# Optimization experiments

Measured on AMD Instinct MI355X. Metric: run time of the kernel, lower is better.

Reference implementation:

```python
import jax, jax.numpy as jnp
import numpy as np

B, T, F, H = 64, 1024, 160, 1024


def setup_inputs() -> dict:
    key = jax.random.key(0)
    ks = jax.random.split(key, 18)
    s = lambda k, shape, scale=0.05: (jax.random.normal(k, shape, jnp.float32) * scale)
    inp = {
        "x": jax.random.normal(ks[0], (B, T, F), jnp.float32),
        # encoder GRU layer 0 (input F -> hidden H), PyTorch gate order r,z,n
        "Wih0": s(ks[1], (3 * H, F)), "Whh0": s(ks[2], (3 * H, H)),
        "bih0": s(ks[3], (3 * H,)), "bhh0": s(ks[4], (3 * H,)),
        # encoder GRU layer 1 (input H -> hidden H)
        "Wih1": s(ks[5], (3 * H, H)), "Whh1": s(ks[6], (3 * H, H)),
        "bih1": s(ks[7], (3 * H,)), "bhh1": s(ks[8], (3 * H,)),
        # fc: (n_enc_layers*H) -> H
        "fcW": s(ks[9], (H, 2 * H)), "fcb": jnp.zeros((H,), jnp.float32),
        # decoder GRUCell (input F -> hidden H)
        "dWih": s(ks[10], (3 * H, F)), "dWhh": s(ks[11], (3 * H, H)),
        "dbih": s(ks[12], (3 * H,)), "dbhh": s(ks[13], (3 * H,)),
        # dec_proj: H -> F
        "pW": s(ks[14], (F, H)), "pb": jnp.zeros((F,), jnp.float32),
    }
    return inp


def gru_step(h, xt, Wih, Whh, bih, bhh):
    # PyTorch GRU/GRUCell math, gate order (r, z, n)
    gi = xt @ Wih.T + bih          # [B, 3H]
    gh = h @ Whh.T + bhh           # [B, 3H]
    ir, iz, inn = jnp.split(gi, 3, axis=-1)
    hr, hz, hn = jnp.split(gh, 3, axis=-1)
    r = jax.nn.sigmoid(ir + hr)
    z = jax.nn.sigmoid(iz + hz)
    n = jnp.tanh(inn + r * hn)
    return (1.0 - z) * n + z * h


def reference(x, Wih0, Whh0, bih0, bhh0, Wih1, Whh1, bih1, bhh1,
              fcW, fcb, dWih, dWhh, dbih, dbhh, pW, pb):
    Bx, Tx = x.shape[0], x.shape[1]
    xs = jnp.swapaxes(x, 0, 1)  # [T, B, F]

    def run_layer(seq, Wih, Whh, bih, bhh):
        h0 = jnp.zeros((Bx, Whh.shape[1]), x.dtype)
        def step(h, xt):
            h = gru_step(h, xt, Wih, Whh, bih, bhh)
            return h, h
        hT, hs = jax.lax.scan(step, h0, seq)
        return hT, hs

    # 2-layer encoder GRU (dropout disabled: eval-mode / deterministic reference)
    h1, hs0 = run_layer(xs, Wih0, Whh0, bih0, bhh0)
    h2, _ = run_layer(hs0, Wih1, Whh1, bih1, bhh1)

    # h_n permute+view -> concat(layer0, layer1) along features
    h = jnp.tanh(jnp.concatenate([h1, h2], axis=-1) @ fcW.T + fcb)  # [B, H]

    i0 = jnp.zeros((Bx, pW.shape[0]), x.dtype)
    def dec_step(carry, _):
        hd, i = carry
        hd = gru_step(hd, i, dWih, dWhh, dbih, dbhh)
        i = hd @ pW.T + pb
        return (hd, i), i
    _, outs = jax.lax.scan(dec_step, (h, i0), None, length=Tx)  # [T, B, F]
    return jnp.swapaxes(outs, 0, 1)  # [B, T, F]
```

## Files before the change

kernel.cpp:

```cpp
#include <hip/hip_runtime.h>
#include <math.h>

#define NWG 256
#define NTH 512

typedef _Float16 f16;
typedef __attribute__((ext_vector_type(8))) _Float16 h8;
typedef __attribute__((ext_vector_type(4))) float f4;

namespace {
constexpr int T_ = 1024, F_ = 160, H_ = 1024;
constexpr float SC = 2048.f;
constexpr float INV = 1.f / 2048.f;

constexpr int ESLOTH = 512 * 64 * 8;
constexpr int DSLOTH = 256 * 64 * 8;
constexpr int ELO = 256;
constexpr int DLO = 128;

constexpr size_t WS_BAR  = 0;
constexpr size_t WS_CVEC = 4096;
constexpr size_t WS_WDEC = 16384;
constexpr size_t WS_ENCA = WS_WDEC + (size_t)4 * H_ * H_ * 4;
constexpr size_t WS_DECA = WS_ENCA + (size_t)2 * ESLOTH * 2;
constexpr size_t WS_STRM = WS_DECA + (size_t)2 * DSLOTH * 2;

constexpr int DBUF_B = 135168;
constexpr int TBUF_B = DBUF_B + 17408;
constexpr int ZP_B   = TBUF_B + 2048;
constexpr int LDS_B  = ZP_B + 64;
}

__device__ __forceinline__ f4 MF(h8 a, h8 b, f4 c) {
  return __builtin_amdgcn_mfma_f32_16x16x32_f16(a, b, c, 0, 0, 0);
}

__device__ __forceinline__ void fsplit(float v, f16& hi, f16& lo) {
  const float hf = (fabsf(v) >= 6.103515625e-05f) ? (float)(f16)v : 0.f;
  hi = (f16)hf;
  lo = (f16)((v - hf) * SC);
}

__device__ __forceinline__ void gbar(unsigned* bar, int wg, unsigned& phase) {
  __syncthreads();
  ++phase;
  if (threadIdx.x == 0) {
    unsigned* grp = bar + ((wg >> 4) << 5);
    unsigned old = __hip_atomic_fetch_add(grp, 1u, __ATOMIC_ACQ_REL, __HIP_MEMORY_SCOPE_AGENT);
    if ((old & 15u) == 15u) {
      unsigned r = __hip_atomic_fetch_add(bar + 512, 1u, __ATOMIC_ACQ_REL, __HIP_MEMORY_SCOPE_AGENT);
      if ((r & 15u) == 15u)
        __hip_atomic_fetch_add(bar + 544, 1u, __ATOMIC_ACQ_REL, __HIP_MEMORY_SCOPE_AGENT);
    }
    while (__hip_atomic_load(bar + 544, __ATOMIC_RELAXED, __HIP_MEMORY_SCOPE_AGENT) < phase)
      __builtin_amdgcn_s_sleep(1);
    (void)__hip_atomic_load(bar + 544, __ATOMIC_ACQUIRE, __HIP_MEMORY_SCOPE_AGENT);
  }
  __syncthreads();
}

__device__ void stageEnc(f16* __restrict__ whi, f16* __restrict__ wlo,
                         const float* __restrict__ Wx, const float* __restrict__ Wh,
                         int KX, int XOo, int KO, int u0, int tid) {
  for (int task = tid; task < KO * 24; task += NTH) {
    const int oct = task / 24;
    const int sl = task - oct * 24;
    const int g = (sl < 16) ? (sl >> 3) : 2;
    const int u = u0 + (sl & 7);
    const float* src = (oct < XOo)
        ? (Wx + (size_t)(g * H_ + u) * KX + (size_t)oct * 8)
        : (Wh + (size_t)(g * H_ + u) * H_ + (size_t)(oct - XOo) * 8);
    const float4 a = *(const float4*)src;
    const float4 b = *(const float4*)(src + 4);
    const float v[8] = {a.x, a.y, a.z, a.w, b.x, b.y, b.z, b.w};
    h8 hv, lv;
#pragma unroll
    for (int e = 0; e < 8; ++e) { f16 hh, ll; fsplit(v[e], hh, ll); hv[e] = hh; lv[e] = ll; }
    *(h8*)(whi + ((size_t)oct * 25 + sl) * 8) = hv;
    if (wlo) *(h8*)(wlo + ((size_t)oct * 25 + sl) * 8) = lv;
  }
}

__device__ void stageDec(f16* __restrict__ whi, f16* __restrict__ wlo,
                         const float* __restrict__ wdec, const float* __restrict__ dWhh,
                         int u0, int tid, bool t1set) {
  for (int task = tid; task < 128 * 32; task += NTH) {
    const int oct = task >> 5, sl = task & 31;
    const int g = sl >> 3;
    const int u = u0 + (sl & 7);
    float v[8];
    if (t1set) {
      if (g == 2) {
#pragma unroll
        for (int e = 0; e < 8; ++e) v[e] = 0.f;
      } else {
        const float* s = dWhh + (size_t)((g == 3 ? 2 : g) * H_ + u) * H_ + (size_t)oct * 8;
        const float4 a = *(const float4*)s, b = *(const float4*)(s + 4);
        v[0]=a.x; v[1]=a.y; v[2]=a.z; v[3]=a.w; v[4]=b.x; v[5]=b.y; v[6]=b.z; v[7]=b.w;
      }
    } else {
      const float* s = wdec + (size_t)(g * H_ + u) * H_ + (size_t)oct * 8;
      const float4 a = *(const float4*)s, b = *(const float4*)(s + 4);
      v[0]=a.x; v[1]=a.y; v[2]=a.z; v[3]=a.w; v[4]=b.x; v[5]=b.y; v[6]=b.z; v[7]=b.w;
    }
    h8 hv, lv;
#pragma unroll
    for (int e = 0; e < 8; ++e) { f16 hh, ll; fsplit(v[e], hh, ll); hv[e] = hh; lv[e] = ll; }
    *(h8*)(whi + ((size_t)oct * 33 + sl) * 8) = hv;
    *(h8*)(wlo + ((size_t)oct * 33 + sl) * 8) = lv;
  }
}

__device__ void stageProj(f16* __restrict__ whi, f16* __restrict__ wlo,
                          const float* __restrict__ pW, int f0, int tid) {
  for (int task = tid; task < 128 * 16; task += NTH) {
    const int oct = task >> 4, sl = task & 15;
    const float* s = pW + (size_t)(f0 + sl) * H_ + (size_t)oct * 8;
    const float4 a = *(const float4*)s, b = *(const float4*)(s + 4);
    const float v[8] = {a.x, a.y, a.z, a.w, b.x, b.y, b.z, b.w};
    h8 hv, lv;
#pragma unroll
    for (int e = 0; e < 8; ++e) { f16 hh, ll; fsplit(v[e], hh, ll); hv[e] = hh; lv[e] = ll; }
    *(h8*)(whi + ((size_t)oct * 17 + sl) * 8) = hv;
    *(h8*)(wlo + ((size_t)oct * 17 + sl) * 8) = lv;
  }
}

template<int NT, bool NSPLIT, int ROWH, bool STRM>
__device__ __forceinline__ void gmm(f4* Dh, f4* Dc,
    const f16* __restrict__ Ab, int aoctBase, int loOct,
    const f16* __restrict__ whi, const f16* __restrict__ wlo,
    const f16* __restrict__ strm,
    int ktn, int octBase, int XO, int ls, int lq, int lane,
    const f16* __restrict__ zp) {
  auto LD = [&](int kk, h8& ah, h8& al, h8& bh0, h8& bl0, h8& bh1, h8& bl1) {
    const int aoct = aoctBase + kk * 4 + lq;
    ah = *(const h8*)(Ab + (size_t)aoct * 512);
    al = *(const h8*)(Ab + (size_t)(aoct + loOct) * 512);
    const int oct = octBase + kk * 4 + lq;
    bh0 = *(const h8*)(whi + ((size_t)oct * ROWH + ls) * 8);
    if constexpr (STRM) bl0 = *(const h8*)(strm + ((size_t)(kk * 2) * 64 + lane) * 8);
    else bl0 = *(const h8*)(wlo + ((size_t)oct * ROWH + ls) * 8);
    if constexpr (NT == 2) {
      bool act = true; int psl;
      if constexpr (NSPLIT) { act = (ls < 8) ? (oct < XO) : (oct >= XO); psl = 16 + (ls & 7); }
      else { psl = 16 + ls; }
      bh1 = *(const h8*)(act ? (whi + ((size_t)oct * ROWH + psl) * 8) : zp);
      if constexpr (STRM) bl1 = *(const h8*)(strm + ((size_t)(kk * 2 + 1) * 64 + lane) * 8);
      else bl1 = *(const h8*)(act ? (wlo + ((size_t)oct * ROWH + psl) * 8) : zp);
    }
  };
  h8 ah, al, bh0, bl0, bh1, bl1;
  LD(0, ah, al, bh0, bl0, bh1, bl1);
  for (int kk = 0; kk < ktn; ++kk) {
    h8 ah2, al2, bh02, bl02, bh12, bl12;
    const int nk = (kk + 1 < ktn) ? (kk + 1) : kk;
    LD(nk, ah2, al2, bh02, bl02, bh12, bl12);
    Dh[0] = MF(ah, bh0, Dh[0]);
    Dc[0] = MF(al, bh0, Dc[0]);
    Dc[0] = MF(ah, bl0, Dc[0]);
    if constexpr (NT == 2) {
      Dh[1] = MF(ah, bh1, Dh[1]);
      Dc[1] = MF(al, bh1, Dc[1]);
      Dc[1] = MF(ah, bl1, Dc[1]);
    }
    ah = ah2; al = al2; bh0 = bh02; bl0 = bl02;
    if constexpr (NT == 2) { bh1 = bh12; bl1 = bl12; }
  }
}

__device__ __forceinline__ void gmm_x(f4* Dh, f4* Dc, const float* __restrict__ xp,
    const f16* __restrict__ whi, const f16* __restrict__ wlo,
    int ls, int lq, const f16* __restrict__ zp) {
#pragma unroll
  for (int kk = 0; kk < 5; ++kk) {
    const float4 a = *(const float4*)(xp + kk * 32);
    const float4 b = *(const float4*)(xp + kk * 32 + 4);
    const float v[8] = {a.x, a.y, a.z, a.w, b.x, b.y, b.z, b.w};
    h8 ah, al;
#pragma unroll
    for (int e = 0; e < 8; ++e) { f16 hh, ll; fsplit(v[e], hh, ll); ah[e] = hh; al[e] = ll; }
    const int oct = kk * 4 + lq;
    {
      const h8 bh2 = *(const h8*)(whi + ((size_t)oct * 25 + ls) * 8);
      const h8 bl2 = *(const h8*)(wlo + ((size_t)oct * 25 + ls) * 8);
      Dh[0] = MF(ah, bh2, Dh[0]);
      Dc[0] = MF(al, bh2, Dc[0]);
      Dc[0] = MF(ah, bl2, Dc[0]);
    }
    {
      const bool act = (ls < 8);
      const int psl = 16 + (ls & 7);
      const h8 bh2 = *(const h8*)(act ? (whi + ((size_t)oct * 25 + psl) * 8) : zp);
      const h8 bl2 = *(const h8*)(act ? (wlo + ((size_t)oct * 25 + psl) * 8) : zp);
      Dh[1] = MF(ah, bh2, Dh[1]);
      Dc[1] = MF(al, bh2, Dc[1]);
      Dc[1] = MF(ah, bl2, Dc[1]);
    }
  }
}

__global__ void build_c_kernel(const float* __restrict__ dWih, const float* __restrict__ dbih,
                               const float* __restrict__ pb, float* __restrict__ cvec) {
  const int r = blockIdx.x * 256 + threadIdx.x;
  if (r >= 3 * H_) return;
  float a = dbih[r];
  for (int f = 0; f < F_; ++f) a += dWih[(size_t)r * F_ + f] * pb[f];
  cvec[r] = a;
}

__global__ void build_wdec_kernel(const float* __restrict__ dWih, const float* __restrict__ dWhh,
                                  const float* __restrict__ pW, float* __restrict__ wdec) {
  const int idx = blockIdx.x * 256 + threadIdx.x;
  if (idx >= 3 * H_ * 128) return;
  const int row = idx >> 7;
  const int oct = idx & 127;
  float v[8] = {0, 0, 0, 0, 0, 0, 0, 0};
  const float* wr = dWih + (size_t)row * F_;
  for (int f = 0; f < F_; ++f) {
    const float w = wr[f];
    const float4 p0 = *(const float4*)(pW + (size_t)f * H_ + oct * 8);
    const float4 p1 = *(const float4*)(pW + (size_t)f * H_ + oct * 8 + 4);
    v[0] += w * p0.x; v[1] += w * p0.y; v[2] += w * p0.z; v[3] += w * p0.w;
    v[4] += w * p1.x; v[5] += w * p1.y; v[6] += w * p1.z; v[7] += w * p1.w;
  }
  if ((row >> 10) < 2) {
    const float* hr = dWhh + (size_t)row * H_ + oct * 8;
#pragma unroll
    for (int e = 0; e < 8; ++e) v[e] += hr[e];
  }
  float* o = wdec + (size_t)row * H_ + oct * 8;
#pragma unroll
  for (int e = 0; e < 8; ++e) o[e] = v[e];
}
__global__ void build_wdec_nh(const float* __restrict__ dWhh, float* __restrict__ wdec) {
  const int idx = blockIdx.x * 256 + threadIdx.x;
  if (idx >= H_ * H_) return;
  wdec[(size_t)3 * H_ * H_ + idx] = dWhh[(size_t)2 * H_ * H_ + idx];
}

__global__ void build_strm(const float* __restrict__ Wih1, const float* __restrict__ Whh1,
                           f16* __restrict__ strm) {
  const size_t idx = (size_t)blockIdx.x * 256 + threadIdx.x;
  const int j = (int)(idx & 7);
  const int lane = (int)((idx >> 3) & 63);
  const int nt = (int)((idx >> 9) & 1);
  const int kk = (int)((idx >> 10) & 31);
  const int kb = (int)((idx >> 15) & 1);
  const int wg = (int)(idx >> 16);
  const int c = lane & 15, lq = lane >> 4;
  const int oct = kb * 128 + kk * 4 + lq;
  const int k = oct * 8 + j;
  float v = 0.f;
  if (nt == 0) {
    const int row = (c >> 3) * H_ + wg * 8 + (c & 7);
    v = (oct < 128) ? Wih1[(size_t)row * H_ + k] : Whh1[(size_t)row * H_ + (k - 1024)];
  } else {
    const bool act = (c < 8) ? (oct < 128) : (oct >= 128);
    if (act) {
      const int row = 2 * H_ + wg * 8 + (c & 7);
      v = (oct < 128) ? Wih1[(size_t)row * H_ + k] : Whh1[(size_t)row * H_ + (k - 1024)];
    }
  }
  f16 hh, ll; fsplit(v, hh, ll);
  strm[idx] = ll;
}

__global__ void __launch_bounds__(NTH, 1) speech_ae_persistent(
    const float* __restrict__ x,
    const float* __restrict__ Wih0, const float* __restrict__ Whh0,
    const float* __restrict__ bih0, const float* __restrict__ bhh0,
    const float* __restrict__ Wih1, const float* __restrict__ Whh1,
    const float* __restrict__ bih1, const float* __restrict__ bhh1,
    const float* __restrict__ fcW, const float* __restrict__ fcb,
    const float* __restrict__ dbih, const float* __restrict__ dbhh,
    const float* __restrict__ pW, const float* __restrict__ pb,
    const float* __restrict__ dWhh,
    float* __restrict__ out, void* ws) {
  extern __shared__ char ldsb[];
  f16* wh = (f16*)ldsb;
  float* dbuf = (float*)(ldsb + DBUF_B);
  float* tbuf = (float*)(ldsb + TBUF_B);
  f16* zp = (f16*)(ldsb + ZP_B);

  char* wsb = (char*)ws;
  unsigned* bar = (unsigned*)(wsb + WS_BAR);
  const float* cvec = (const float*)(wsb + WS_CVEC);
  const float* wdec = (const float*)(wsb + WS_WDEC);
  f16* encA = (f16*)(wsb + WS_ENCA);
  f16* decA = (f16*)(wsb + WS_DECA);
  const f16* strm = (const f16*)(wsb + WS_STRM);

  const int tid = threadIdx.x, wg = blockIdx.x;
  const int lane = tid & 63, wv = tid >> 6;
  const int ls = lane & 15, lq = lane >> 4;
  const int m0 = (wv & 3) * 16, kb = wv >> 2;
  const int mb = m0 + ls;
  const bool isL1 = (wg < 128);
  unsigned phase = 0;
  const f16* strmW = strm + (size_t)(wg * 2 + kb) * 32768;

  const float* bi = isL1 ? bih1 : bih0;
  const float* bh_ = isL1 ? bhh1 : bhh0;
  const int eru = (isL1 ? wg * 8 : (wg - 128) * 8) + wv;
  const float ebr = bi[eru] + bh_[eru];
  const float ebz = bi[H_ + eru] + bh_[H_ + eru];
  const float ebni = bi[2 * H_ + eru];
  const float ebnh = bh_[2 * H_ + eru];
  float hreg = 0.f;

  float b1r = 0, b1z = 0, b1ni = 0, b1nh = 0, bfr = 0, bfz = 0, bfni = 0, bfnh = 0, hdreg = 0.f;
  if (wg < 128) {
    const int rw = wg * 8 + wv;
    b1r = dbih[rw] + dbhh[rw];
    b1z = dbih[H_ + rw] + dbhh[H_ + rw];
    b1ni = dbih[2 * H_ + rw];
    b1nh = dbhh[2 * H_ + rw];
    bfr = cvec[rw] + dbhh[rw];
    bfz = cvec[H_ + rw] + dbhh[H_ + rw];
    bfni = cvec[2 * H_ + rw];
    bfnh = dbhh[2 * H_ + rw];
  }
  const int f0 = (wg - 128) * 16;
  float pbr[4] = {0, 0, 0, 0};
  if (wg >= 128 && wg < 138 && tid < 256) {
    const int fq = tid & 3;
#pragma unroll
    for (int e = 0; e < 4; ++e) pbr[e] = pb[f0 + fq * 4 + e];
  }

  if (isL1) stageEnc(wh, nullptr, Wih1, Whh1, H_, 128, 256, wg * 8, tid);
  else stageEnc(wh, wh + 29600, Wih0, Whh0, F_, 20, 148, (wg - 128) * 8, tid);
  if (tid < 16) zp[tid] = (f16)0.f;
  __syncthreads();

  for (int s = 0; s <= T_; ++s) {
    const bool active = isL1 ? (s >= 1) : (s < T_);
    if (active) {
      const int t = isL1 ? (s - 1) : s;
      f4 Dh[2] = {{0.f,0.f,0.f,0.f},{0.f,0.f,0.f,0.f}};
      f4 Dc[2] = {{0.f,0.f,0.f,0.f},{0.f,0.f,0.f,0.f}};
      if (isL1) {
        if (kb == 0) {
          const f16* Ab = encA + (size_t)(t & 1) * ESLOTH + (size_t)mb * 8;
          gmm<2, true, 25, true>(Dh, Dc, Ab, 0, ELO, wh, nullptr, strmW, 32, 0, 128, ls, lq, lane, zp);
        } else if (t >= 1) {
          const f16* Ab = encA + (size_t)((t - 1) & 1) * ESLOTH + (size_t)mb * 8;
          gmm<2, true, 25, true>(Dh, Dc, Ab, 128, ELO, wh, nullptr, strmW, 32, 128, 128, ls, lq, lane, zp);
        }
      } else {
        if (kb == 0) {
          const float* xp = x + ((size_t)mb * T_ + t) * F_ + lq * 8;
          gmm_x(Dh, Dc, xp, wh, wh + 29600, ls, lq, zp);
          if (t >= 1) {
            const f16* Ab = encA + (size_t)((t - 1) & 1) * ESLOTH + (size_t)mb * 8;
            gmm<2, true, 25, false>(Dh, Dc, Ab, 0, ELO, wh, wh + 29600, nullptr, 14, 20, 20, ls, lq, lane, zp);
          }
        } else if (t >= 1) {
          const f16* Ab = encA + (size_t)((t - 1) & 1) * ESLOTH + (size_t)mb * 8;
          gmm<2, true, 25, false>(Dh, Dc, Ab, 56, ELO, wh, wh + 29600, nullptr, 18, 76, 20, ls, lq, lane, zp);
        }
      }
      *(f4*)(dbuf + kb * 2176 + ls * 68 + m0 + lq * 4) = Dh[0] + Dc[0] * INV;
      *(f4*)(dbuf + kb * 2176 + (16 + ls) * 68 + m0 + lq * 4) = Dh[1] + Dc[1] * INV;
      __syncthreads();
      const int b = lane;
      const float gr  = dbuf[wv * 68 + b]        + dbuf[2176 + wv * 68 + b]        + ebr;
      const float gz  = dbuf[(8 + wv) * 68 + b]  + dbuf[2176 + (8 + wv) * 68 + b]  + ebz;
      const float gni = dbuf[(16 + wv) * 68 + b] + dbuf[2176 + (16 + wv) * 68 + b] + ebni;
      const float gnh = dbuf[(24 + wv) * 68 + b] + dbuf[2176 + (24 + wv) * 68 + b] + ebnh;
      const float rg = 1.f / (1.f + expf(-gr));
      const float zg = 1.f / (1.f + expf(-gz));
      const float ng = tanhf(gni + rg * gnh);
      const float hn = (1.f - zg) * ng + zg * hreg;
      hreg = hn;
      tbuf[wv * 64 + b] = hn;
      __syncthreads();
      if (tid < 64) {
        const int oct = isL1 ? (128 + wg) : (wg - 128);
        f16* dst = encA + (size_t)(t & 1) * ESLOTH + ((size_t)oct * 64 + tid) * 8;
        h8 hv, lv;
#pragma unroll
        for (int e = 0; e < 8; ++e) { f16 hh, ll; fsplit(tbuf[e * 64 + tid], hh, ll); hv[e] = hh; lv[e] = ll; }
        *(h8*)dst = hv;
        *(h8*)(dst + (size_t)ELO * 512) = lv;
      }
    }
    gbar(bar, wg, phase);
  }

  if (wg < 128) {
    const int u0f = wg * 8;
    const int b = lane;
    float acc[8] = {0, 0, 0, 0, 0, 0, 0, 0};
    for (int ko = wv * 32; ko < wv * 32 + 32; ++ko) {
      const f16* hp = encA + ESLOTH + ((size_t)ko * 64 + b) * 8;
      const h8 hiv = *(const h8*)hp;
      const h8 lov = *(const h8*)(hp + (size_t)ELO * 512);
      float hv[8];
#pragma unroll
      for (int e = 0; e < 8; ++e) hv[e] = (float)hiv[e] + (float)lov[e] * INV;
#pragma unroll
      for (int u = 0; u < 8; ++u) {
        const float* wr = fcW + (size_t)(u0f + u) * 2048 + (size_t)ko * 8;
        const float4 wa = *(const float4*)wr, wb = *(const float4*)(wr + 4);
        acc[u] += hv[0] * wa.x + hv[1] * wa.y + hv[2] * wa.z + hv[3] * wa.w
                + hv[4] * wb.x + hv[5] * wb.y + hv[6] * wb.z + hv[7] * wb.w;
      }
    }
    __syncthreads();
#pragma unroll
    for (int u = 0; u < 8; ++u) dbuf[(u * 8 + wv) * 68 + b] = acc[u];
    __syncthreads();
    float sum = fcb[u0f + wv];
#pragma unroll
    for (int g = 0; g < 8; ++g) sum += dbuf[(wv * 8 + g) * 68 + lane];
    tbuf[wv * 64 + lane] = tanhf(sum);
    __syncthreads();
    if (tid < 64) {
      f16* dst = decA + ((size_t)wg * 64 + tid) * 8;
      h8 hv, lv;
#pragma unroll
      for (int e = 0; e < 8; ++e) { f16 hh, ll; fsplit(tbuf[e * 64 + tid], hh, ll); hv[e] = hh; lv[e] = ll; }
      *(h8*)dst = hv;
      *(h8*)(dst + (size_t)DLO * 512) = lv;
    }
  }
  if (wg < 128) stageDec(wh, wh + 33792, nullptr, dWhh, wg * 8, tid, true);
  else if (wg < 138) stageProj(wh, wh + 17408, pW, f0, tid);
  gbar(bar, wg, phase);

  auto dec_step = [&](int t, bool first) {
    f4 Dh[2] = {{0.f,0.f,0.f,0.f},{0.f,0.f,0.f,0.f}};
    f4 Dc[2] = {{0.f,0.f,0.f,0.f},{0.f,0.f,0.f,0.f}};
    const f16* Ab = decA + (size_t)((t - 1) & 1) * DSLOTH + (size_t)mb * 8;
    gmm<2, false, 33, false>(Dh, Dc, Ab, kb * 64, DLO, wh, wh + 33792, nullptr, 16, kb * 64, 0, ls, lq, lane, zp);
    *(f4*)(dbuf + kb * 2176 + ls * 68 + m0 + lq * 4) = Dh[0] + Dc[0] * INV;
    *(f4*)(dbuf + kb * 2176 + (16 + ls) * 68 + m0 + lq * 4) = Dh[1] + Dc[1] * INV;
    __syncthreads();
    const int b = lane;
    const float hprev = first ? tbuf[wv * 64 + b] : hdreg;
    const float gr  = dbuf[wv * 68 + b]        + dbuf[2176 + wv * 68 + b]        + (first ? b1r : bfr);
    const float gz  = dbuf[(8 + wv) * 68 + b]  + dbuf[2176 + (8 + wv) * 68 + b]  + (first ? b1z : bfz);
    const float gni = dbuf[(16 + wv) * 68 + b] + dbuf[2176 + (16 + wv) * 68 + b] + (first ? b1ni : bfni);
    const float gnh = dbuf[(24 + wv) * 68 + b] + dbuf[2176 + (24 + wv) * 68 + b] + (first ? b1nh : bfnh);
    const float rg = 1.f / (1.f + expf(-gr));
    const float zg = 1.f / (1.f + expf(-gz));
    const float ng = tanhf(gni + rg * gnh);
    const float hn = (1.f - zg) * ng + zg * hprev;
    hdreg = hn;
    tbuf[wv * 64 + b] = hn;
    __syncthreads();
    if (tid < 64) {
      f16* dst = decA + (size_t)(t & 1) * DSLOTH + ((size_t)wg * 64 + tid) * 8;
      h8 hv, lv;
#pragma unroll
      for (int e = 0; e < 8; ++e) { f16 hh, ll; fsplit(tbuf[e * 64 + tid], hh, ll); hv[e] = hh; lv[e] = ll; }
      *(h8*)dst = hv;
      *(h8*)(dst + (size_t)DLO * 512) = lv;
    }
  };

  auto proj = [&](int t2) {
    f4 Dh[1] = {{0.f,0.f,0.f,0.f}};
    f4 Dc[1] = {{0.f,0.f,0.f,0.f}};
    const f16* Ab = decA + (size_t)((t2 - 1) & 1) * DSLOTH + (size_t)mb * 8;
    gmm<1, false, 17, false>(Dh, Dc, Ab, kb * 64, DLO, wh, wh + 17408, nullptr, 16, kb * 64, 0, ls, lq, lane, zp);
    *(f4*)(dbuf + kb * 2176 + ls * 68 + m0 + lq * 4) = Dh[0] + Dc[0] * INV;
    __syncthreads();
    if (tid < 256) {
      const int b2 = tid >> 2, fq = tid & 3;
      float4 o;
      o.x = dbuf[(fq * 4 + 0) * 68 + b2] + dbuf[2176 + (fq * 4 + 0) * 68 + b2] + pbr[0];
      o.y = dbuf[(fq * 4 + 1) * 68 + b2] + dbuf[2176 + (fq * 4 + 1) * 68 + b2] + pbr[1];
      o.z = dbuf[(fq * 4 + 2) * 68 + b2] + dbuf[2176 + (fq * 4 + 2) * 68 + b2] + pbr[2];
      o.w = dbuf[(fq * 4 + 3) * 68 + b2] + dbuf[2176 + (fq * 4 + 3) * 68 + b2] + pbr[3];
      *(float4*)(out + (size_t)b2 * (T_ * F_) + (size_t)(t2 - 2) * F_ + f0 + fq * 4) = o;
    }
  };

  if (wg < 128) dec_step(1, true);
  gbar(bar, wg, phase);
  if (wg < 128) {
    stageDec(wh, wh + 33792, wdec, nullptr, wg * 8, tid, false);
    __syncthreads();
  }

  for (int t2 = 2; t2 <= T_ + 1; ++t2) {
    if (wg < 128) {
      if (t2 <= T_) dec_step(t2, false);
    } else if (wg < 138) {
      proj(t2);
    }
    gbar(bar, wg, phase);
  }
}

extern "C" void kernel_launch(void* const* d_in, const int* in_sizes, int n_in,
                              void* d_out, int out_size, void* d_ws, size_t ws_size,
                              hipStream_t stream) {
  (void)in_sizes; (void)n_in; (void)out_size; (void)ws_size;
  const float* x    = (const float*)d_in[0];
  const float* Wih0 = (const float*)d_in[1];
  const float* Whh0 = (const float*)d_in[2];
  const float* bih0 = (const float*)d_in[3];
  const float* bhh0 = (const float*)d_in[4];
  const float* Wih1 = (const float*)d_in[5];
  const float* Whh1 = (const float*)d_in[6];
  const float* bih1 = (const float*)d_in[7];
  const float* bhh1 = (const float*)d_in[8];
  const float* fcW  = (const float*)d_in[9];
  const float* fcb  = (const float*)d_in[10];
  const float* dWih = (const float*)d_in[11];
  const float* dWhh = (const float*)d_in[12];
  const float* dbih = (const float*)d_in[13];
  const float* dbhh = (const float*)d_in[14];
  const float* pW   = (const float*)d_in[15];
  const float* pb   = (const float*)d_in[16];
  float* out = (float*)d_out;
  char* wsb = (char*)d_ws;

  hipFuncSetAttribute((const void*)speech_ae_persistent,
                      hipFuncAttributeMaxDynamicSharedMemorySize, LDS_B);
  hipMemsetAsync(d_ws, 0, 4096, stream);
  build_c_kernel<<<(3 * H_ + 255) / 256, 256, 0, stream>>>(dWih, dbih, pb, (float*)(wsb + WS_CVEC));
  build_wdec_kernel<<<(3 * H_ * 128 + 255) / 256, 256, 0, stream>>>(dWih, dWhh, pW, (float*)(wsb + WS_WDEC));
  build_wdec_nh<<<(H_ * H_ + 255) / 256, 256, 0, stream>>>(dWhh, (float*)(wsb + WS_WDEC));
  build_strm<<<32768, 256, 0, stream>>>(Wih1, Whh1, (f16*)(wsb + WS_STRM));
  speech_ae_persistent<<<NWG, NTH, LDS_B, stream>>>(
      x, Wih0, Whh0, bih0, bhh0, Wih1, Whh1, bih1, bhh1, fcW, fcb,
      dbih, dbhh, pW, pb, dWhh, out, d_ws);
}
```

Measured before the change: 40.11 ms.

## Double workgroup threads to split GEMM K-range four ways with LDS combine

Raises the block size from 512 to 1024 threads so each workgroup runs 16 waves. The K dimension of every recurrent GEMM (encoder layers, decoder cell, projection) is split into four quarters instead of two. Partial results are merged through a two-phase LDS add using an extra barrier. This is meant to shorten the per-timestep critical path of the serial recurrence, at the cost of extra __syncthreads, more LDS traffic, and possible register pressure from 1024-thread blocks.

New measurement: 48.11 ms. 19.9% more time.

```diff
diff --git a/kernel.cpp b/kernel.cpp
--- a/kernel.cpp
+++ b/kernel.cpp
@@ -2,7 +2,7 @@
 #include <math.h>
 
 #define NWG 256
-#define NTH 512
+#define NTH 1024
 
 typedef _Float16 f16;
 typedef __attribute__((ext_vector_type(8))) _Float16 h8;
@@ -294,15 +294,17 @@
   const int tid = threadIdx.x, wg = blockIdx.x;
   const int lane = tid & 63, wv = tid >> 6;
   const int ls = lane & 15, lq = lane >> 4;
-  const int m0 = (wv & 3) * 16, kb = wv >> 2;
+  const int m0 = (wv & 3) * 16;
+  const int kq = wv >> 2;
   const int mb = m0 + ls;
+  const int uv = wv & 7;
   const bool isL1 = (wg < 128);
   unsigned phase = 0;
-  const f16* strmW = strm + (size_t)(wg * 2 + kb) * 32768;
+  const f16* strmQ = strm + (size_t)(wg * 2 + (kq >> 1)) * 32768 + (size_t)(kq & 1) * 16384;
 
   const float* bi = isL1 ? bih1 : bih0;
   const float* bh_ = isL1 ? bhh1 : bhh0;
-  const int eru = (isL1 ? wg * 8 : (wg - 128) * 8) + wv;
+  const int eru = (isL1 ? wg * 8 : (wg - 128) * 8) + uv;
   const float ebr = bi[eru] + bh_[eru];
   const float ebz = bi[H_ + eru] + bh_[H_ + eru];
   const float ebni = bi[2 * H_ + eru];
@@ -311,7 +313,7 @@
 
   float b1r = 0, b1z = 0, b1ni = 0, b1nh = 0, bfr = 0, bfz = 0, bfni = 0, bfnh = 0, hdreg = 0.f;
   if (wg < 128) {
-    const int rw = wg * 8 + wv;
+    const int rw = wg * 8 + uv;
     b1r = dbih[rw] + dbhh[rw];
     b1z = dbih[H_ + rw] + dbhh[H_ + rw];
     b1ni = dbih[2 * H_ + rw];
@@ -334,6 +336,22 @@
   if (tid < 16) zp[tid] = (f16)0.f;
   __syncthreads();
 
+  auto combine2 = [&](const f4& r0, const f4& r1, bool two) {
+    float* dp = dbuf + (kq & 1) * 2176;
+    f4* p0 = (f4*)(dp + ls * 68 + m0 + lq * 4);
+    f4* p1 = (f4*)(dp + (16 + ls) * 68 + m0 + lq * 4);
+    if (kq < 2) {
+      *p0 = r0;
+      if (two) *p1 = r1;
+    }
+    __syncthreads();
+    if (kq >= 2) {
+      *p0 = *p0 + r0;
+      if (two) *p1 = *p1 + r1;
+    }
+    __syncthreads();
+  };
+
   for (int s = 0; s <= T_; ++s) {
     const bool active = isL1 ? (s >= 1) : (s < T_);
     if (active) {
@@ -341,40 +359,41 @@
       f4 Dh[2] = {{0.f,0.f,0.f,0.f},{0.f,0.f,0.f,0.f}};
       f4 Dc[2] = {{0.f,0.f,0.f,0.f},{0.f,0.f,0.f,0.f}};
       if (isL1) {
-        if (kb == 0) {
+        if (kq < 2) {
           const f16* Ab = encA + (size_t)(t & 1) * ESLOTH + (size_t)mb * 8;
-          gmm<2, true, 25, true>(Dh, Dc, Ab, 0, ELO, wh, nullptr, strmW, 32, 0, 128, ls, lq, lane, zp);
+          gmm<2, true, 25, true>(Dh, Dc, Ab, kq * 64, ELO, wh, nullptr, strmQ, 16, kq * 64, 128, ls, lq, lane, zp);
         } else if (t >= 1) {
           const f16* Ab = encA + (size_t)((t - 1) & 1) * ESLOTH + (size_t)mb * 8;
-          gmm<2, true, 25, true>(Dh, Dc, Ab, 128, ELO, wh, nullptr, strmW, 32, 128, 128, ls, lq, lane, zp);
+          const int ob = 128 + (kq - 2) * 64;
+          gmm<2, true, 25, true>(Dh, Dc, Ab, ob, ELO, wh, nullptr, strmQ, 16, ob, 128, ls, lq, lane, zp);
         }
       } else {
-        if (kb == 0) {
+        const f16* Ab = encA + (size_t)((s - 1) & 1) * ESLOTH + (size_t)mb * 8;
+        if (kq == 0) {
           const float* xp = x + ((size_t)mb * T_ + t) * F_ + lq * 8;
           gmm_x(Dh, Dc, xp, wh, wh + 29600, ls, lq, zp);
-          if (t >= 1) {
-            const f16* Ab = encA + (size_t)((t - 1) & 1) * ESLOTH + (size_t)mb * 8;
-            gmm<2, true, 25, false>(Dh, Dc, Ab, 0, ELO, wh, wh + 29600, nullptr, 14, 20, 20, ls, lq, lane, zp);
-          }
+          if (t >= 1)
+            gmm<2, true, 25, false>(Dh, Dc, Ab, 0, ELO, wh, wh + 29600, nullptr, 4, 20, 20, ls, lq, lane, zp);
         } else if (t >= 1) {
-          const f16* Ab = encA + (size_t)((t - 1) & 1) * ESLOTH + (size_t)mb * 8;
-          gmm<2, true, 25, false>(Dh, Dc, Ab, 56, ELO, wh, wh + 29600, nullptr, 18, 76, 20, ls, lq, lane, zp);
+          const int ao = (kq == 1) ? 16 : (kq == 2) ? 52 : 88;
+          const int kt = (kq == 3) ? 10 : 9;
+          gmm<2, true, 25, false>(Dh, Dc, Ab, ao, ELO, wh, wh + 29600, nullptr, kt, 20 + ao, 20, ls, lq, lane, zp);
         }
       }
-      *(f4*)(dbuf + kb * 2176 + ls * 68 + m0 + lq * 4) = Dh[0] + Dc[0] * INV;
-      *(f4*)(dbuf + kb * 2176 + (16 + ls) * 68 + m0 + lq * 4) = Dh[1] + Dc[1] * INV;
-      __syncthreads();
-      const int b = lane;
-      const float gr  = dbuf[wv * 68 + b]        + dbuf[2176 + wv * 68 + b]        + ebr;
-      const float gz  = dbuf[(8 + wv) * 68 + b]  + dbuf[2176 + (8 + wv) * 68 + b]  + ebz;
-      const float gni = dbuf[(16 + wv) * 68 + b] + dbuf[2176 + (16 + wv) * 68 + b] + ebni;
-      const float gnh = dbuf[(24 + wv) * 68 + b] + dbuf[2176 + (24 + wv) * 68 + b] + ebnh;
-      const float rg = 1.f / (1.f + expf(-gr));
-      const float zg = 1.f / (1.f + expf(-gz));
-      const float ng = tanhf(gni + rg * gnh);
-      const float hn = (1.f - zg) * ng + zg * hreg;
-      hreg = hn;
-      tbuf[wv * 64 + b] = hn;
+      combine2(Dh[0] + Dc[0] * INV, Dh[1] + Dc[1] * INV, true);
+      if (tid < 512) {
+        const int b = lane;
+        const float gr  = dbuf[uv * 68 + b]        + dbuf[2176 + uv * 68 + b]        + ebr;
+        const float gz  = dbuf[(8 + uv) * 68 + b]  + dbuf[2176 + (8 + uv) * 68 + b]  + ebz;
+        const float gni = dbuf[(16 + uv) * 68 + b] + dbuf[2176 + (16 + uv) * 68 + b] + ebni;
+        const float gnh = dbuf[(24 + uv) * 68 + b] + dbuf[2176 + (24 + uv) * 68 + b] + ebnh;
+        const float rg = 1.f / (1.f + expf(-gr));
+        const float zg = 1.f / (1.f + expf(-gz));
+        const float ng = tanhf(gni + rg * gnh);
+        const float hn = (1.f - zg) * ng + zg * hreg;
+        hreg = hn;
+        tbuf[uv * 64 + b] = hn;
+      }
       __syncthreads();
       if (tid < 64) {
         const int oct = isL1 ? (128 + wg) : (wg - 128);
@@ -393,29 +412,35 @@
     const int u0f = wg * 8;
     const int b = lane;
     float acc[8] = {0, 0, 0, 0, 0, 0, 0, 0};
-    for (int ko = wv * 32; ko < wv * 32 + 32; ++ko) {
-      const f16* hp = encA + ESLOTH + ((size_t)ko * 64 + b) * 8;
-      const h8 hiv = *(const h8*)hp;
-      const h8 lov = *(const h8*)(hp + (size_t)ELO * 512);
-      float hv[8];
-#pragma unroll
-      for (int e = 0; e < 8; ++e) hv[e] = (float)hiv[e] + (float)lov[e] * INV;
-#pragma unroll
-      for (int u = 0; u < 8; ++u) {
-        const float* wr = fcW + (size_t)(u0f + u) * 2048 + (size_t)ko * 8;
-        const float4 wa = *(const float4*)wr, wb = *(const float4*)(wr + 4);
-        acc[u] += hv[0] * wa.x + hv[1] * wa.y + hv[2] * wa.z + hv[3] * wa.w
-                + hv[4] * wb.x + hv[5] * wb.y + hv[6] * wb.z + hv[7] * wb.w;
+    if (wv < 8) {
+      for (int ko = wv * 32; ko < wv * 32 + 32; ++ko) {
+        const f16* hp = encA + ESLOTH + ((size_t)ko * 64 + b) * 8;
+        const h8 hiv = *(const h8*)hp;
+        const h8 lov = *(const h8*)(hp + (size_t)ELO * 512);
+        float hv[8];
+#pragma unroll
+        for (int e = 0; e < 8; ++e) hv[e] = (float)hiv[e] + (float)lov[e] * INV;
+#pragma unroll
+        for (int u = 0; u < 8; ++u) {
+          const float* wr = fcW + (size_t)(u0f + u) * 2048 + (size_t)ko * 8;
+          const float4 wa = *(const float4*)wr, wb = *(const float4*)(wr + 4);
+          acc[u] += hv[0] * wa.x + hv[1] * wa.y + hv[2] * wa.z + hv[3] * wa.w
+                  + hv[4] * wb.x + hv[5] * wb.y + hv[6] * wb.z + hv[7] * wb.w;
+        }
       }
     }
     __syncthreads();
-#pragma unroll
-    for (int u = 0; u < 8; ++u) dbuf[(u * 8 + wv) * 68 + b] = acc[u];
-    __syncthreads();
-    float sum = fcb[u0f + wv];
-#pragma unroll
-    for (int g = 0; g < 8; ++g) sum += dbuf[(wv * 8 + g) * 68 + lane];
-    tbuf[wv * 64 + lane] = tanhf(sum);
+    if (wv < 8) {
+#pragma unroll
+      for (int u = 0; u < 8; ++u) dbuf[(u * 8 + wv) * 68 + b] = acc[u];
+    }
+    __syncthreads();
+    if (tid < 512) {
+      float sum = fcb[u0f + uv];
+#pragma unroll
+      for (int g = 0; g < 8; ++g) sum += dbuf[(uv * 8 + g) * 68 + lane];
+      tbuf[uv * 64 + lane] = tanhf(sum);
+    }
     __syncthreads();
     if (tid < 64) {
       f16* dst = decA + ((size_t)wg * 64 + tid) * 8;
@@ -434,22 +459,22 @@
     f4 Dh[2] = {{0.f,0.f,0.f,0.f},{0.f,0.f,0.f,0.f}};
     f4 Dc[2] = {{0.f,0.f,0.f,0.f},{0.f,0.f,0.f,0.f}};
     const f16* Ab = decA + (size_t)((t - 1) & 1) * DSLOTH + (size_t)mb * 8;
-    gmm<2, false, 33, false>(Dh, Dc, Ab, kb * 64, DLO, wh, wh + 33792, nullptr, 16, kb * 64, 0, ls, lq, lane, zp);
-    *(f4*)(dbuf + kb * 2176 + ls * 68 + m0 + lq * 4) = Dh[0] + Dc[0] * INV;
-    *(f4*)(dbuf + kb * 2176 + (16 + ls) * 68 + m0 + lq * 4) = Dh[1] + Dc[1] * INV;
-    __syncthreads();
-    const int b = lane;
-    const float hprev = first ? tbuf[wv * 64 + b] : hdreg;
-    const float gr  = dbuf[wv * 68 + b]        + dbuf[2176 + wv * 68 + b]        + (first ? b1r : bfr);
-    const float gz  = dbuf[(8 + wv) * 68 + b]  + dbuf[2176 + (8 + wv) * 68 + b]  + (first ? b1z : bfz);
-    const float gni = dbuf[(16 + wv) * 68 + b] + dbuf[2176 + (16 + wv) * 68 + b] + (first ? b1ni : bfni);
-    const float gnh = dbuf[(24 + wv) * 68 + b] + dbuf[2176 + (24 + wv) * 68 + b] + (first ? b1nh : bfnh);
-    const float rg = 1.f / (1.f + expf(-gr));
-    const float zg = 1.f / (1.f + expf(-gz));
-    const float ng = tanhf(gni + rg * gnh);
-    const float hn = (1.f - zg) * ng + zg * hprev;
-    hdreg = hn;
-    tbuf[wv * 64 + b] = hn;
+    gmm<2, false, 33, false>(Dh, Dc, Ab, kq * 32, DLO, wh, wh + 33792, nullptr, 8, kq * 32, 0, ls, lq, lane, zp);
+    combine2(Dh[0] + Dc[0] * INV, Dh[1] + Dc[1] * INV, true);
+    if (tid < 512) {
+      const int b = lane;
+      const float hprev = first ? tbuf[uv * 64 + b] : hdreg;
+      const float gr  = dbuf[uv * 68 + b]        + dbuf[2176 + uv * 68 + b]        + (first ? b1r : bfr);
+      const float gz  = dbuf[(8 + uv) * 68 + b]  + dbuf[2176 + (8 + uv) * 68 + b]  + (first ? b1z : bfz);
+      const float gni = dbuf[(16 + uv) * 68 + b] + dbuf[2176 + (16 + uv) * 68 + b] + (first ? b1ni : bfni);
+      const float gnh = dbuf[(24 + uv) * 68 + b] + dbuf[2176 + (24 + uv) * 68 + b] + (first ? b1nh : bfnh);
+      const float rg = 1.f / (1.f + expf(-gr));
+      const float zg = 1.f / (1.f + expf(-gz));
+      const float ng = tanhf(gni + rg * gnh);
+      const float hn = (1.f - zg) * ng + zg * hprev;
+      hdreg = hn;
+      tbuf[uv * 64 + b] = hn;
+    }
     __syncthreads();
     if (tid < 64) {
       f16* dst = decA + (size_t)(t & 1) * DSLOTH + ((size_t)wg * 64 + tid) * 8;
@@ -465,9 +490,9 @@
     f4 Dh[1] = {{0.f,0.f,0.f,0.f}};
     f4 Dc[1] = {{0.f,0.f,0.f,0.f}};
     const f16* Ab = decA + (size_t)((t2 - 1) & 1) * DSLOTH + (size_t)mb * 8;
-    gmm<1, false, 17, false>(Dh, Dc, Ab, kb * 64, DLO, wh, wh + 17408, nullptr, 16, kb * 64, 0, ls, lq, lane, zp);
-    *(f4*)(dbuf + kb * 2176 + ls * 68 + m0 + lq * 4) = Dh[0] + Dc[0] * INV;
-    __syncthreads();
+    gmm<1, false, 17, false>(Dh, Dc, Ab, kq * 32, DLO, wh, wh + 17408, nullptr, 8, kq * 32, 0, ls, lq, lane, zp);
+    f4 dummy = {0.f, 0.f, 0.f, 0.f};
+    combine2(Dh[0] + Dc[0] * INV, dummy, false);
     if (tid < 256) {
       const int b2 = tid >> 2, fq = tid & 3;
       float4 o;
```
